# Optimization experiments

Hardware: AMD Instinct MI355X
Metric: run time of the kernel (lower is better)

Reference implementation:

```python
import jax, jax.numpy as jnp
import numpy as np

B, D, C = 16384, 1024, 2048

def setup_inputs() -> dict:
    key = jax.random.key(0)
    k1, k2 = jax.random.split(key)
    x = jax.random.normal(k1, (B, D), dtype=jnp.float32)
    # kaiming_normal_ with nonlinearity='relu': std = sqrt(2 / fan_in)
    W = jax.random.normal(k2, (C, D), dtype=jnp.float32) * jnp.sqrt(2.0 / D)
    return {"x": x, "W": W, "task_id": 0}

def reference(x, W, task_id):
    # Original: -(x[:, :, None] - W.T[None, :, :])**2 .mean(1)  -> [B, C]
    # Algebraic rewrite: -(||x||^2/D - 2*x.W^T/D + ||w||^2/D)
    d = jnp.asarray(x.shape[1], x.dtype)
    x2 = jnp.sum(x * x, axis=1, keepdims=True) / d          # [B, 1]
    w2 = jnp.sum(W * W, axis=1) / d                          # [C]
    cross = jnp.einsum('bd,cd->bc', x, W) * (2.0 / d)        # [B, C]
    return cross - x2 - w2[None, :]
```

## Files before the change

kernel.cpp:

```cpp
#include <hip/hip_runtime.h>
#include <hip/hip_bf16.h>
#include <stdint.h>

#define B_ROWS 16384
#define D_DIM  1024
#define C_DIM  2048
#define KT32   (D_DIM / 32)
#define MT_TOT (B_ROWS / 16)
#define NT_TOT (C_DIM  / 16)

typedef short bf16x8 __attribute__((ext_vector_type(8)));
typedef float f32x4  __attribute__((ext_vector_type(4)));

#define AS1 __attribute__((address_space(1)))
#define AS3 __attribute__((address_space(3)))
#define BARRIER __builtin_amdgcn_s_barrier()
#define LGKM0 asm volatile("s_waitcnt lgkmcnt(0)")
#define VMCNT(n) asm volatile("s_waitcnt vmcnt(" #n ")" ::: "memory")
#define PRIO1 __builtin_amdgcn_s_setprio(1)
#define PRIO0 __builtin_amdgcn_s_setprio(0)

__global__ __launch_bounds__(256) void pack_norm(
        const float* __restrict__ x, const float* __restrict__ W,
        ushort* __restrict__ Apk, ushort* __restrict__ Bpk,
        float* __restrict__ x2, float* __restrict__ w2) {
    int chunk = blockIdx.x * 4 + (threadIdx.x >> 6);
    const int lane = threadIdx.x & 63;
    const int XCH = MT_TOT * KT32;
    const float* src; ushort* dst; float* norm;
    if (chunk < XCH) { src = x; dst = Apk; norm = x2; }
    else             { src = W; dst = Bpk; norm = w2; chunk -= XCH; }
    const int tile = chunk >> 5;
    const int kt   = chunk & 31;

    const int row = tile * 16 + (lane & 15);
    const int k0  = kt * 32 + (lane >> 4) * 8;
    const float4 v0 = *(const float4*)(src + (size_t)row * D_DIM + k0);
    const float4 v1 = *(const float4*)(src + (size_t)row * D_DIM + k0 + 4);
    float s = v0.x*v0.x + v0.y*v0.y + v0.z*v0.z + v0.w*v0.w
            + v1.x*v1.x + v1.y*v1.y + v1.z*v1.z + v1.w*v1.w;

    ushort u[8]; __hip_bfloat16 h;
    h = __float2bfloat16(v0.x); u[0] = *(const ushort*)&h;
    h = __float2bfloat16(v0.y); u[1] = *(const ushort*)&h;
    h = __float2bfloat16(v0.z); u[2] = *(const ushort*)&h;
    h = __float2bfloat16(v0.w); u[3] = *(const ushort*)&h;
    h = __float2bfloat16(v1.x); u[4] = *(const ushort*)&h;
    h = __float2bfloat16(v1.y); u[5] = *(const ushort*)&h;
    h = __float2bfloat16(v1.z); u[6] = *(const ushort*)&h;
    h = __float2bfloat16(v1.w); u[7] = *(const ushort*)&h;
    *(bf16x8*)(dst + ((size_t)chunk * 64 + lane) * 8) = *(const bf16x8*)u;

    s += __shfl_xor(s, 16, 64);
    s += __shfl_xor(s, 32, 64);
    if (lane < 16) atomicAdd(norm + tile * 16 + lane, s * (1.0f / (float)D_DIM));
}

__global__ __launch_bounds__(256, 3) void gemm_tb(
        const ushort* __restrict__ Apk, const ushort* __restrict__ Bpk,
        const float* __restrict__ x2, const float* __restrict__ w2,
        float* __restrict__ out) {
    __shared__ ushort As[3 * 4096];
    __shared__ ushort Bs[3 * 4096];

    const int tid  = threadIdx.x;
    const int lane = tid & 63;
    const int wv   = tid >> 6;

    const int wid = (blockIdx.x & 7) * 256 + (blockIdx.x >> 3);
    const int bm  = wid >> 4;
    const int bn  = wid & 15;

    const ushort* aSrc = Apk + ((size_t)(bm * 8) * KT32) * 512 + lane * 8;
    const ushort* bSrc = Bpk + ((size_t)(bn * 8) * KT32) * 512 + lane * 8;

    const ushort* aRd = As + (wv >> 1) * 2048 + lane * 8;
    const ushort* bRd = Bs + (wv & 1) * 2048 + lane * 8;

    const int t0 = wv, t1 = wv + 4;

#define STAGE(ktc, bufO) do { \
    __builtin_amdgcn_global_load_lds( \
        (const AS1 void*)(aSrc + ((size_t)t0 * KT32 + (ktc)) * 512), \
        (AS3 void*)(As + (bufO) + t0 * 512), 16, 0, 0); \
    __builtin_amdgcn_global_load_lds( \
        (const AS1 void*)(aSrc + ((size_t)t1 * KT32 + (ktc)) * 512), \
        (AS3 void*)(As + (bufO) + t1 * 512), 16, 0, 0); \
    __builtin_amdgcn_global_load_lds( \
        (const AS1 void*)(bSrc + ((size_t)t0 * KT32 + (ktc)) * 512), \
        (AS3 void*)(Bs + (bufO) + t0 * 512), 16, 0, 0); \
    __builtin_amdgcn_global_load_lds( \
        (const AS1 void*)(bSrc + ((size_t)t1 * KT32 + (ktc)) * 512), \
        (AS3 void*)(Bs + (bufO) + t1 * 512), 16, 0, 0); \
  } while (0)

    f32x4 acc[4][4];
    #pragma unroll
    for (int mi = 0; mi < 4; ++mi)
        #pragma unroll
        for (int ni = 0; ni < 4; ++ni)
            acc[mi][ni] = (f32x4){0.f, 0.f, 0.f, 0.f};

    STAGE(0, 0);
    STAGE(1, 4096);
    VMCNT(4);
    BARRIER;

    int curO = 0, nxtO = 4096, stgO = 8192;
    for (int kt = 0; kt < KT32; ++kt) {
        bf16x8 a[4], b[4];
        #pragma unroll
        for (int mi = 0; mi < 4; ++mi)
            a[mi] = *(const bf16x8*)(aRd + curO + mi * 512);
        #pragma unroll
        for (int ni = 0; ni < 4; ++ni)
            b[ni] = *(const bf16x8*)(bRd + curO + ni * 512);

        STAGE((kt + 2) & 31, stgO);

        VMCNT(4);
        BARRIER;
        LGKM0;
        PRIO1;
        #pragma unroll
        for (int mi = 0; mi < 4; ++mi)
            #pragma unroll
            for (int ni = 0; ni < 4; ++ni)
                acc[mi][ni] = __builtin_amdgcn_mfma_f32_16x16x32_bf16(
                    a[mi], b[ni], acc[mi][ni], 0, 0, 0);
        PRIO0;
        BARRIER;

        const int t = curO; curO = nxtO; nxtO = stgO; stgO = t;
    }

    const float scale = 2.0f / (float)D_DIM;
    const int rsel = lane & 15;
    const int quad = lane >> 4;
    const int mT0  = bm * 8 + (wv >> 1) * 4;
    const int nT0  = bn * 8 + (wv & 1) * 4;
    const int row0 = mT0 * 16 + quad * 4;
    const int col0 = nT0 * 16 + rsel;

    float x2r[4][4];
    #pragma unroll
    for (int mi = 0; mi < 4; ++mi)
        #pragma unroll
        for (int r = 0; r < 4; ++r)
            x2r[mi][r] = x2[row0 + mi * 16 + r];

    #pragma unroll
    for (int ni = 0; ni < 4; ++ni) {
        const int c = col0 + ni * 16;
        const float wc = w2[c];
        #pragma unroll
        for (int mi = 0; mi < 4; ++mi) {
            #pragma unroll
            for (int r = 0; r < 4; ++r) {
                const int rr = row0 + mi * 16 + r;
                out[(size_t)rr * C_DIM + c] = acc[mi][ni][r] * scale - x2r[mi][r] - wc;
            }
        }
    }
#undef STAGE
}

extern "C" void kernel_launch(void* const* d_in, const int* in_sizes, int n_in,
                              void* d_out, int out_size, void* d_ws, size_t ws_size,
                              hipStream_t stream) {
    const float* x = (const float*)d_in[0];
    const float* W = (const float*)d_in[1];
    float* out = (float*)d_out;

    char* ws = (char*)d_ws;
    ushort* Apk = (ushort*)ws;
    ushort* Bpk = (ushort*)(ws + (size_t)B_ROWS * D_DIM * sizeof(ushort));
    float*  x2  = (float*)(ws + (size_t)(B_ROWS + C_DIM) * D_DIM * sizeof(ushort));
    float*  w2  = x2 + B_ROWS;

    hipMemsetAsync(x2, 0, (B_ROWS + C_DIM) * sizeof(float), stream);

    pack_norm<<<(MT_TOT * KT32 + NT_TOT * KT32) / 4, 256, 0, stream>>>(
        x, W, Apk, Bpk, x2, w2);

    gemm_tb<<<(B_ROWS / 128) * (C_DIM / 128), 256, 0, stream>>>(
        Apk, Bpk, x2, w2, out);
}
```

Baseline: 245.8 us.

## Load A fragments directly into registers, keep only B staged in LDS

The GEMM no longer stages the A tile through LDS. Each wave loads its four A fragments straight from global memory into registers, one k-step ahead, double-buffered in register sets and with the loop unrolled by two. Only B still goes through the three-buffer LDS pipeline. This halves LDS traffic and footprint, but every wave pair now fetches its A data from global/L2 separately (two waves share the same A rows), and register pressure rises.

Result: slower. 272.5 us (+10.9%).

```diff
diff --git a/kernel.cpp b/kernel.cpp
--- a/kernel.cpp
+++ b/kernel.cpp
@@ -56,11 +56,10 @@
     if (lane < 16) atomicAdd(norm + tile * 16 + lane, s * (1.0f / (float)D_DIM));
 }
 
-__global__ __launch_bounds__(256, 3) void gemm_tb(
+__global__ __launch_bounds__(256, 3) void gemm_areg(
         const ushort* __restrict__ Apk, const ushort* __restrict__ Bpk,
         const float* __restrict__ x2, const float* __restrict__ w2,
         float* __restrict__ out) {
-    __shared__ ushort As[3 * 4096];
     __shared__ ushort Bs[3 * 4096];
 
     const int tid  = threadIdx.x;
@@ -74,24 +73,20 @@
     const ushort* aSrc = Apk + ((size_t)(bm * 8) * KT32) * 512 + lane * 8;
     const ushort* bSrc = Bpk + ((size_t)(bn * 8) * KT32) * 512 + lane * 8;
 
-    const ushort* aRd = As + (wv >> 1) * 2048 + lane * 8;
+    const int tA = (wv >> 1) * 4;
     const ushort* bRd = Bs + (wv & 1) * 2048 + lane * 8;
 
-    const int t0 = wv, t1 = wv + 4;
-
-#define STAGE(ktc, bufO) do { \
-    __builtin_amdgcn_global_load_lds( \
-        (const AS1 void*)(aSrc + ((size_t)t0 * KT32 + (ktc)) * 512), \
-        (AS3 void*)(As + (bufO) + t0 * 512), 16, 0, 0); \
-    __builtin_amdgcn_global_load_lds( \
-        (const AS1 void*)(aSrc + ((size_t)t1 * KT32 + (ktc)) * 512), \
-        (AS3 void*)(As + (bufO) + t1 * 512), 16, 0, 0); \
-    __builtin_amdgcn_global_load_lds( \
-        (const AS1 void*)(bSrc + ((size_t)t0 * KT32 + (ktc)) * 512), \
-        (AS3 void*)(Bs + (bufO) + t0 * 512), 16, 0, 0); \
-    __builtin_amdgcn_global_load_lds( \
-        (const AS1 void*)(bSrc + ((size_t)t1 * KT32 + (ktc)) * 512), \
-        (AS3 void*)(Bs + (bufO) + t1 * 512), 16, 0, 0); \
+#define GLL(src, dst) __builtin_amdgcn_global_load_lds( \
+        (const AS1 void*)(src), (AS3 void*)(dst), 16, 0, 0)
+#define STAGEB(ktc, bO) do { \
+    GLL(bSrc + ((size_t)(wv)     * KT32 + (ktc)) * 512, Bs + (bO) + (wv)     * 512); \
+    GLL(bSrc + ((size_t)(wv + 4) * KT32 + (ktc)) * 512, Bs + (bO) + (wv + 4) * 512); \
+  } while (0)
+#define LOADA(AR, ktc) do { \
+    AR##0 = *(const bf16x8*)(aSrc + ((size_t)(tA + 0) * KT32 + (ktc)) * 512); \
+    AR##1 = *(const bf16x8*)(aSrc + ((size_t)(tA + 1) * KT32 + (ktc)) * 512); \
+    AR##2 = *(const bf16x8*)(aSrc + ((size_t)(tA + 2) * KT32 + (ktc)) * 512); \
+    AR##3 = *(const bf16x8*)(aSrc + ((size_t)(tA + 3) * KT32 + (ktc)) * 512); \
   } while (0)
 
     f32x4 acc[4][4];
@@ -101,43 +96,57 @@
         for (int ni = 0; ni < 4; ++ni)
             acc[mi][ni] = (f32x4){0.f, 0.f, 0.f, 0.f};
 
-    STAGE(0, 0);
-    STAGE(1, 4096);
-    VMCNT(4);
+    bf16x8 aE0, aE1, aE2, aE3, aO0, aO1, aO2, aO3;
+
+    LOADA(aE, 0);
+    STAGEB(0, 0);
+    STAGEB(1, 4096);
+    VMCNT(2);
     BARRIER;
 
-    int curO = 0, nxtO = 4096, stgO = 8192;
-    for (int kt = 0; kt < KT32; ++kt) {
-        bf16x8 a[4], b[4];
-        #pragma unroll
-        for (int mi = 0; mi < 4; ++mi)
-            a[mi] = *(const bf16x8*)(aRd + curO + mi * 512);
-        #pragma unroll
-        for (int ni = 0; ni < 4; ++ni)
-            b[ni] = *(const bf16x8*)(bRd + curO + ni * 512);
-
-        STAGE((kt + 2) & 31, stgO);
-
-        VMCNT(4);
-        BARRIER;
-        LGKM0;
-        PRIO1;
-        #pragma unroll
-        for (int mi = 0; mi < 4; ++mi)
-            #pragma unroll
-            for (int ni = 0; ni < 4; ++ni)
-                acc[mi][ni] = __builtin_amdgcn_mfma_f32_16x16x32_bf16(
-                    a[mi], b[ni], acc[mi][ni], 0, 0, 0);
-        PRIO0;
-        BARRIER;
-
-        const int t = curO; curO = nxtO; nxtO = stgO; stgO = t;
+    int cB = 0, nB = 4096, sB = 8192;
+
+#define STEP(kt, AC, AN) do { \
+    bf16x8 b0_ = *(const bf16x8*)(bRd + cB);                                  \
+    bf16x8 b1_ = *(const bf16x8*)(bRd + cB + 512);                            \
+    bf16x8 b2_ = *(const bf16x8*)(bRd + cB + 1024);                           \
+    bf16x8 b3_ = *(const bf16x8*)(bRd + cB + 1536);                           \
+    LOADA(AN, ((kt) + 1) & 31);                                               \
+    STAGEB(((kt) + 2) & 31, sB);                                              \
+    VMCNT(6);         \
+    BARRIER;       \
+    LGKM0;                                                                    \
+    PRIO1;                                                                    \
+    acc[0][0] = __builtin_amdgcn_mfma_f32_16x16x32_bf16(AC##0, b0_, acc[0][0], 0, 0, 0); \
+    acc[0][1] = __builtin_amdgcn_mfma_f32_16x16x32_bf16(AC##0, b1_, acc[0][1], 0, 0, 0); \
+    acc[0][2] = __builtin_amdgcn_mfma_f32_16x16x32_bf16(AC##0, b2_, acc[0][2], 0, 0, 0); \
+    acc[0][3] = __builtin_amdgcn_mfma_f32_16x16x32_bf16(AC##0, b3_, acc[0][3], 0, 0, 0); \
+    acc[1][0] = __builtin_amdgcn_mfma_f32_16x16x32_bf16(AC##1, b0_, acc[1][0], 0, 0, 0); \
+    acc[1][1] = __builtin_amdgcn_mfma_f32_16x16x32_bf16(AC##1, b1_, acc[1][1], 0, 0, 0); \
+    acc[1][2] = __builtin_amdgcn_mfma_f32_16x16x32_bf16(AC##1, b2_, acc[1][2], 0, 0, 0); \
+    acc[1][3] = __builtin_amdgcn_mfma_f32_16x16x32_bf16(AC##1, b3_, acc[1][3], 0, 0, 0); \
+    acc[2][0] = __builtin_amdgcn_mfma_f32_16x16x32_bf16(AC##2, b0_, acc[2][0], 0, 0, 0); \
+    acc[2][1] = __builtin_amdgcn_mfma_f32_16x16x32_bf16(AC##2, b1_, acc[2][1], 0, 0, 0); \
+    acc[2][2] = __builtin_amdgcn_mfma_f32_16x16x32_bf16(AC##2, b2_, acc[2][2], 0, 0, 0); \
+    acc[2][3] = __builtin_amdgcn_mfma_f32_16x16x32_bf16(AC##2, b3_, acc[2][3], 0, 0, 0); \
+    acc[3][0] = __builtin_amdgcn_mfma_f32_16x16x32_bf16(AC##3, b0_, acc[3][0], 0, 0, 0); \
+    acc[3][1] = __builtin_amdgcn_mfma_f32_16x16x32_bf16(AC##3, b1_, acc[3][1], 0, 0, 0); \
+    acc[3][2] = __builtin_amdgcn_mfma_f32_16x16x32_bf16(AC##3, b2_, acc[3][2], 0, 0, 0); \
+    acc[3][3] = __builtin_amdgcn_mfma_f32_16x16x32_bf16(AC##3, b3_, acc[3][3], 0, 0, 0); \
+    PRIO0;                                                                    \
+    BARRIER;         \
+    int t_ = cB; cB = nB; nB = sB; sB = t_;                                   \
+  } while (0)
+
+    for (int kt = 0; kt < KT32; kt += 2) {
+        STEP(kt,     aE, aO);
+        STEP(kt + 1, aO, aE);
     }
 
     const float scale = 2.0f / (float)D_DIM;
     const int rsel = lane & 15;
     const int quad = lane >> 4;
-    const int mT0  = bm * 8 + (wv >> 1) * 4;
+    const int mT0  = bm * 8 + tA;
     const int nT0  = bn * 8 + (wv & 1) * 4;
     const int row0 = mT0 * 16 + quad * 4;
     const int col0 = nT0 * 16 + rsel;
@@ -162,7 +171,10 @@
             }
         }
     }
-#undef STAGE
+#undef STEP
+#undef LOADA
+#undef STAGEB
+#undef GLL
 }
 
 extern "C" void kernel_launch(void* const* d_in, const int* in_sizes, int n_in,
@@ -183,6 +195,6 @@
     pack_norm<<<(MT_TOT * KT32 + NT_TOT * KT32) / 4, 256, 0, stream>>>(
         x, W, Apk, Bpk, x2, w2);
 
-    gemm_tb<<<(B_ROWS / 128) * (C_DIM / 128), 256, 0, stream>>>(
+    gemm_areg<<<(B_ROWS / 128) * (C_DIM / 128), 256, 0, stream>>>(
         Apk, Bpk, x2, w2, out);
 }
```

## Restructure pack kernel to coalesced row reads with LDS swizzled transpose

Applied to the files above, without the earlier changes.

The fp32-to-bf16 pack kernel now assigns one block per 16-row tile and reads each row fully contiguously, then stages the bf16 values through a swizzled LDS buffer before writing the MFMA-packed layout. This replaces the old per-chunk scattered 32-byte reads with fully coalesced loads, and cuts norm atomics to one per row per block. It adds an LDS round trip, a barrier and more shuffle reductions per row.

Result: slower. 265.2 us (+7.9%).

```diff
diff --git a/kernel.cpp b/kernel.cpp
--- a/kernel.cpp
+++ b/kernel.cpp
@@ -11,6 +11,7 @@
 
 typedef short bf16x8 __attribute__((ext_vector_type(8)));
 typedef float f32x4  __attribute__((ext_vector_type(4)));
+typedef unsigned short us4 __attribute__((ext_vector_type(4)));
 
 #define AS1 __attribute__((address_space(1)))
 #define AS3 __attribute__((address_space(3)))
@@ -20,40 +21,58 @@
 #define PRIO1 __builtin_amdgcn_s_setprio(1)
 #define PRIO0 __builtin_amdgcn_s_setprio(0)
 
-__global__ __launch_bounds__(256) void pack_norm(
+__global__ __launch_bounds__(256) void pack_norm2(
         const float* __restrict__ x, const float* __restrict__ W,
         ushort* __restrict__ Apk, ushort* __restrict__ Bpk,
         float* __restrict__ x2, float* __restrict__ w2) {
-    int chunk = blockIdx.x * 4 + (threadIdx.x >> 6);
-    const int lane = threadIdx.x & 63;
-    const int XCH = MT_TOT * KT32;
+    __shared__ ushort L[KT32 * 512];
+
+    int tile = blockIdx.x;
     const float* src; ushort* dst; float* norm;
-    if (chunk < XCH) { src = x; dst = Apk; norm = x2; }
-    else             { src = W; dst = Bpk; norm = w2; chunk -= XCH; }
-    const int tile = chunk >> 5;
-    const int kt   = chunk & 31;
-
-    const int row = tile * 16 + (lane & 15);
-    const int k0  = kt * 32 + (lane >> 4) * 8;
-    const float4 v0 = *(const float4*)(src + (size_t)row * D_DIM + k0);
-    const float4 v1 = *(const float4*)(src + (size_t)row * D_DIM + k0 + 4);
-    float s = v0.x*v0.x + v0.y*v0.y + v0.z*v0.z + v0.w*v0.w
-            + v1.x*v1.x + v1.y*v1.y + v1.z*v1.z + v1.w*v1.w;
-
-    ushort u[8]; __hip_bfloat16 h;
-    h = __float2bfloat16(v0.x); u[0] = *(const ushort*)&h;
-    h = __float2bfloat16(v0.y); u[1] = *(const ushort*)&h;
-    h = __float2bfloat16(v0.z); u[2] = *(const ushort*)&h;
-    h = __float2bfloat16(v0.w); u[3] = *(const ushort*)&h;
-    h = __float2bfloat16(v1.x); u[4] = *(const ushort*)&h;
-    h = __float2bfloat16(v1.y); u[5] = *(const ushort*)&h;
-    h = __float2bfloat16(v1.z); u[6] = *(const ushort*)&h;
-    h = __float2bfloat16(v1.w); u[7] = *(const ushort*)&h;
-    *(bf16x8*)(dst + ((size_t)chunk * 64 + lane) * 8) = *(const bf16x8*)u;
-
-    s += __shfl_xor(s, 16, 64);
-    s += __shfl_xor(s, 32, 64);
-    if (lane < 16) atomicAdd(norm + tile * 16 + lane, s * (1.0f / (float)D_DIM));
+    if (tile < MT_TOT) { src = x; dst = Apk; norm = x2; }
+    else               { src = W; dst = Bpk; norm = w2; tile -= MT_TOT; }
+
+    const int t    = threadIdx.x;
+    const int lane = t & 63;
+    const int wv   = t >> 6;
+    const float* tb = src + (size_t)tile * 16 * D_DIM;
+
+    const int kt  = t >> 3;
+    const int s0  = 16 * ((t & 7) >> 1);
+    const int sub = (t & 1) * 4;
+    const int xs  = kt & 7;
+
+    #pragma unroll 4
+    for (int i = 0; i < 16; ++i) {
+        const float4 v = *(const float4*)(tb + i * D_DIM + t * 4);
+        float ls = v.x*v.x + v.y*v.y + v.z*v.z + v.w*v.w;
+
+        ushort u[4]; __hip_bfloat16 h;
+        h = __float2bfloat16(v.x); u[0] = *(const ushort*)&h;
+        h = __float2bfloat16(v.y); u[1] = *(const ushort*)&h;
+        h = __float2bfloat16(v.z); u[2] = *(const ushort*)&h;
+        h = __float2bfloat16(v.w); u[3] = *(const ushort*)&h;
+        const int sp = (i + s0) ^ xs;
+        *(us4*)(L + kt * 512 + sp * 8 + sub) = *(const us4*)u;
+
+        ls += __shfl_xor(ls, 1,  64);
+        ls += __shfl_xor(ls, 2,  64);
+        ls += __shfl_xor(ls, 4,  64);
+        ls += __shfl_xor(ls, 8,  64);
+        ls += __shfl_xor(ls, 16, 64);
+        ls += __shfl_xor(ls, 32, 64);
+        if (lane == 0)
+            atomicAdd(norm + tile * 16 + i, ls * (1.0f / (float)D_DIM));
+    }
+    __syncthreads();
+
+    ushort* dchunk = dst + (size_t)tile * KT32 * 512;
+    #pragma unroll
+    for (int j = 0; j < 8; ++j) {
+        const int c = wv * 8 + j;
+        const bf16x8 g = *(const bf16x8*)(L + c * 512 + (lane ^ (c & 7)) * 8);
+        *(bf16x8*)(dchunk + (size_t)c * 512 + lane * 8) = g;
+    }
 }
 
 __global__ __launch_bounds__(256, 3) void gemm_tb(
@@ -180,7 +199,7 @@
 
     hipMemsetAsync(x2, 0, (B_ROWS + C_DIM) * sizeof(float), stream);
 
-    pack_norm<<<(MT_TOT * KT32 + NT_TOT * KT32) / 4, 256, 0, stream>>>(
+    pack_norm2<<<MT_TOT + NT_TOT, 256, 0, stream>>>(
         x, W, Apk, Bpk, x2, w2);
 
     gemm_tb<<<(B_ROWS / 128) * (C_DIM / 128), 256, 0, stream>>>(
```

## Pack operands row-major per wave and drop norm atomics and memset

Applied to the files above, without the earlier changes.

The pre-pass now has one wave per row. It converts the row to bf16 in plain row-major layout and writes its squared norm directly, so the atomics and the memset launch are gone. The GEMM's global-to-LDS loads now gather from row-major data: each lane reads 16 bytes from a different row with a 2KB stride, where before each wave read a contiguous 1KB pre-tiled block. This removes an extra launch and atomic traffic. The cost is less coalesced loads in the main GEMM loop.

Result: slower. 306.6 us (+24.8%).

```diff
diff --git a/kernel.cpp b/kernel.cpp
--- a/kernel.cpp
+++ b/kernel.cpp
@@ -6,11 +6,10 @@
 #define D_DIM  1024
 #define C_DIM  2048
 #define KT32   (D_DIM / 32)
-#define MT_TOT (B_ROWS / 16)
-#define NT_TOT (C_DIM  / 16)
 
 typedef short bf16x8 __attribute__((ext_vector_type(8)));
 typedef float f32x4  __attribute__((ext_vector_type(4)));
+typedef unsigned short us4 __attribute__((ext_vector_type(4)));
 
 #define AS1 __attribute__((address_space(1)))
 #define AS3 __attribute__((address_space(3)))
@@ -20,44 +19,47 @@
 #define PRIO1 __builtin_amdgcn_s_setprio(1)
 #define PRIO0 __builtin_amdgcn_s_setprio(0)
 
-__global__ __launch_bounds__(256) void pack_norm(
+__device__ __forceinline__ float sq4(f32x4 v) {
+    return v[0]*v[0] + v[1]*v[1] + v[2]*v[2] + v[3]*v[3];
+}
+
+__global__ __launch_bounds__(256) void pack_rows(
         const float* __restrict__ x, const float* __restrict__ W,
-        ushort* __restrict__ Apk, ushort* __restrict__ Bpk,
+        ushort* __restrict__ Abf, ushort* __restrict__ Bbf,
         float* __restrict__ x2, float* __restrict__ w2) {
-    int chunk = blockIdx.x * 4 + (threadIdx.x >> 6);
+    int row = blockIdx.x * 4 + (threadIdx.x >> 6);
     const int lane = threadIdx.x & 63;
-    const int XCH = MT_TOT * KT32;
     const float* src; ushort* dst; float* norm;
-    if (chunk < XCH) { src = x; dst = Apk; norm = x2; }
-    else             { src = W; dst = Bpk; norm = w2; chunk -= XCH; }
-    const int tile = chunk >> 5;
-    const int kt   = chunk & 31;
+    if (row < B_ROWS) { src = x; dst = Abf; norm = x2; }
+    else { row -= B_ROWS; src = W; dst = Bbf; norm = w2; }
 
-    const int row = tile * 16 + (lane & 15);
-    const int k0  = kt * 32 + (lane >> 4) * 8;
-    const float4 v0 = *(const float4*)(src + (size_t)row * D_DIM + k0);
-    const float4 v1 = *(const float4*)(src + (size_t)row * D_DIM + k0 + 4);
-    float s = v0.x*v0.x + v0.y*v0.y + v0.z*v0.z + v0.w*v0.w
-            + v1.x*v1.x + v1.y*v1.y + v1.z*v1.z + v1.w*v1.w;
+    const float* rp = src + (size_t)row * D_DIM;
+    ushort*      wp = dst + (size_t)row * D_DIM;
 
-    ushort u[8]; __hip_bfloat16 h;
-    h = __float2bfloat16(v0.x); u[0] = *(const ushort*)&h;
-    h = __float2bfloat16(v0.y); u[1] = *(const ushort*)&h;
-    h = __float2bfloat16(v0.z); u[2] = *(const ushort*)&h;
-    h = __float2bfloat16(v0.w); u[3] = *(const ushort*)&h;
-    h = __float2bfloat16(v1.x); u[4] = *(const ushort*)&h;
-    h = __float2bfloat16(v1.y); u[5] = *(const ushort*)&h;
-    h = __float2bfloat16(v1.z); u[6] = *(const ushort*)&h;
-    h = __float2bfloat16(v1.w); u[7] = *(const ushort*)&h;
-    *(bf16x8*)(dst + ((size_t)chunk * 64 + lane) * 8) = *(const bf16x8*)u;
-
+    float s = 0.f;
+    #pragma unroll
+    for (int p = 0; p < 4; ++p) {
+        const int o = (p * 64 + lane) * 4;
+        const f32x4 v = *(const f32x4*)(rp + o);
+        s += sq4(v);
+        ushort u[4]; __hip_bfloat16 h;
+        h = __float2bfloat16(v[0]); u[0] = *(const ushort*)&h;
+        h = __float2bfloat16(v[1]); u[1] = *(const ushort*)&h;
+        h = __float2bfloat16(v[2]); u[2] = *(const ushort*)&h;
+        h = __float2bfloat16(v[3]); u[3] = *(const ushort*)&h;
+        *(us4*)(wp + o) = *(const us4*)u;
+    }
+    s += __shfl_xor(s, 1,  64);
+    s += __shfl_xor(s, 2,  64);
+    s += __shfl_xor(s, 4,  64);
+    s += __shfl_xor(s, 8,  64);
     s += __shfl_xor(s, 16, 64);
     s += __shfl_xor(s, 32, 64);
-    if (lane < 16) atomicAdd(norm + tile * 16 + lane, s * (1.0f / (float)D_DIM));
+    if (lane == 0) norm[row] = s * (1.0f / (float)D_DIM);
 }
 
 __global__ __launch_bounds__(256, 3) void gemm_tb(
-        const ushort* __restrict__ Apk, const ushort* __restrict__ Bpk,
+        const ushort* __restrict__ Abf, const ushort* __restrict__ Bbf,
         const float* __restrict__ x2, const float* __restrict__ w2,
         float* __restrict__ out) {
     __shared__ ushort As[3 * 4096];
@@ -71,8 +73,8 @@
     const int bm  = wid >> 4;
     const int bn  = wid & 15;
 
-    const ushort* aSrc = Apk + ((size_t)(bm * 8) * KT32) * 512 + lane * 8;
-    const ushort* bSrc = Bpk + ((size_t)(bn * 8) * KT32) * 512 + lane * 8;
+    const ushort* aSrc = Abf + (size_t)(bm * 128 + (lane & 15)) * D_DIM + (lane >> 4) * 8;
+    const ushort* bSrc = Bbf + (size_t)(bn * 128 + (lane & 15)) * D_DIM + (lane >> 4) * 8;
 
     const ushort* aRd = As + (wv >> 1) * 2048 + lane * 8;
     const ushort* bRd = Bs + (wv & 1) * 2048 + lane * 8;
@@ -81,16 +83,16 @@
 
 #define STAGE(ktc, bufO) do { \
     __builtin_amdgcn_global_load_lds( \
-        (const AS1 void*)(aSrc + ((size_t)t0 * KT32 + (ktc)) * 512), \
+        (const AS1 void*)(aSrc + (size_t)t0 * 16 * D_DIM + (ktc) * 32), \
         (AS3 void*)(As + (bufO) + t0 * 512), 16, 0, 0); \
     __builtin_amdgcn_global_load_lds( \
-        (const AS1 void*)(aSrc + ((size_t)t1 * KT32 + (ktc)) * 512), \
+        (const AS1 void*)(aSrc + (size_t)t1 * 16 * D_DIM + (ktc) * 32), \
         (AS3 void*)(As + (bufO) + t1 * 512), 16, 0, 0); \
     __builtin_amdgcn_global_load_lds( \
-        (const AS1 void*)(bSrc + ((size_t)t0 * KT32 + (ktc)) * 512), \
+        (const AS1 void*)(bSrc + (size_t)t0 * 16 * D_DIM + (ktc) * 32), \
         (AS3 void*)(Bs + (bufO) + t0 * 512), 16, 0, 0); \
     __builtin_amdgcn_global_load_lds( \
-        (const AS1 void*)(bSrc + ((size_t)t1 * KT32 + (ktc)) * 512), \
+        (const AS1 void*)(bSrc + (size_t)t1 * 16 * D_DIM + (ktc) * 32), \
         (AS3 void*)(Bs + (bufO) + t1 * 512), 16, 0, 0); \
   } while (0)
 
@@ -173,16 +175,14 @@
     float* out = (float*)d_out;
 
     char* ws = (char*)d_ws;
-    ushort* Apk = (ushort*)ws;
-    ushort* Bpk = (ushort*)(ws + (size_t)B_ROWS * D_DIM * sizeof(ushort));
+    ushort* Abf = (ushort*)ws;
+    ushort* Bbf = (ushort*)(ws + (size_t)B_ROWS * D_DIM * sizeof(ushort));
     float*  x2  = (float*)(ws + (size_t)(B_ROWS + C_DIM) * D_DIM * sizeof(ushort));
     float*  w2  = x2 + B_ROWS;
 
-    hipMemsetAsync(x2, 0, (B_ROWS + C_DIM) * sizeof(float), stream);
-
-    pack_norm<<<(MT_TOT * KT32 + NT_TOT * KT32) / 4, 256, 0, stream>>>(
-        x, W, Apk, Bpk, x2, w2);
+    pack_rows<<<(B_ROWS + C_DIM) / 4, 256, 0, stream>>>(
+        x, W, Abf, Bbf, x2, w2);
 
     gemm_tb<<<(B_ROWS / 128) * (C_DIM / 128), 256, 0, stream>>>(
-        Apk, Bpk, x2, w2, out);
+        Abf, Bbf, x2, w2, out);
 }
```
